# Kernel optimization log

Hardware: AMD Instinct MI355X
Metric: run time of the kernel (lower is better)

The kernel has to match this reference:

```python
import jax, jax.numpy as jnp
import numpy as np

LMAX = 2
C1 = 64; C2 = 64; COUT = 64
B = 4096
SUM_RDIM = sum(3**L for L in range(LMAX + 1))   # 13
FEAT1 = C1 * SUM_RDIM                            # 832
FEAT2 = C2 * SUM_RDIM


def _enumerate_paths(Lmax):
    paths = []
    for L1 in range(Lmax + 1):
        for L2 in range(Lmax + 1):
            for k in range(min(L1, L2) + 1):
                Lout = L1 + L2 - 2 * k
                if 0 <= Lout <= Lmax:
                    paths.append((L1, L2, Lout, k, False))
            if L1 >= 1 and L2 >= 1:
                for k in range(min(L1 - 1, L2 - 1) + 1):
                    Lout = L1 + L2 - 2 * k - 1
                    if 0 <= Lout <= Lmax:
                        paths.append((L1, L2, Lout, k, True))
    return paths

PATHS = _enumerate_paths(LMAX)   # 15 paths for Lmax=2


def _path_eq(L1, L2, k, use_eps):
    # Fused equation: W[c,a,b] contracted together with the delta/eps path einsum.
    letters = list('defghijklmnopqrstuvwxyz')  # a,b,c reserved for channels
    i_idx = letters[:L1]
    j_idx = letters[L1:L1 + L2]
    for r in range(k):  # delta: contract last k indices of A with last k of B
        j_idx[L2 - k + r] = i_idx[L1 - k + r]
    i_free = i_idx[:L1 - k]
    j_free = j_idx[:L2 - k]
    eps_sub = None
    if use_eps:  # consume last free index of each side via eps_{p i j}
        p = letters[L1 + L2]
        eps_sub = p + i_free[-1] + j_free[-1]
        i_free, j_free = i_free[:-1], j_free[:-1]
        out = i_free + j_free + [p]
    else:
        out = i_free + j_free
    terms = ['cab', '...a' + ''.join(i_idx), '...b' + ''.join(j_idx)]
    if eps_sub is not None:
        terms.append(eps_sub)
    return ','.join(terms) + '->...c' + ''.join(out)


def _epsilon():
    e = np.zeros((3, 3, 3), dtype=np.float32)
    e[0, 1, 2] = e[1, 2, 0] = e[2, 0, 1] = 1.0
    e[2, 1, 0] = e[1, 0, 2] = e[0, 2, 1] = -1.0
    return jnp.asarray(e)


def _split_by_rank(x, C, Lmax):
    batch = x.shape[:-1]
    out, idx = {}, 0
    for L in range(Lmax + 1):
        d = C * 3**L
        blk = x[..., idx:idx + d]
        idx += d
        out[L] = blk.reshape(*batch, C) if L == 0 else blk.reshape(*batch, C, *((3,) * L))
    return out


def setup_inputs() -> dict:
    key = jax.random.key(0)
    k1, k2, k3 = jax.random.split(key, 3)
    x1 = jax.random.normal(k1, (B, FEAT1), dtype=jnp.float32)
    x2 = jax.random.normal(k2, (B, FEAT2), dtype=jnp.float32)
    weight = jax.random.normal(k3, (len(PATHS) * COUT * C1 * C2,), dtype=jnp.float32) * 0.02
    return {"x1": x1, "x2": x2, "weight": weight}


def reference(x1, x2, weight):
    A = _split_by_rank(x1, C1, LMAX)
    Bt = _split_by_rank(x2, C2, LMAX)
    eps = _epsilon().astype(x1.dtype)
    batch = x1.shape[:-1]
    blocks = {L: jnp.zeros((*batch, COUT) + (3,) * L, dtype=x1.dtype) for L in range(LMAX + 1)}
    wsz = COUT * C1 * C2
    for n, (L1, L2, Lout, k, use_eps) in enumerate(PATHS):
        Wp = weight[n * wsz:(n + 1) * wsz].reshape(COUT, C1, C2)
        eq = _path_eq(L1, L2, k, use_eps)
        ops = (Wp, A[L1], Bt[L2]) + ((eps,) if use_eps else ())
        blocks[Lout] = blocks[Lout] + jnp.einsum(eq, *ops, optimize='optimal')
    parts = [blocks[L].reshape(*batch, COUT * 3**L) for L in range(LMAX + 1)]
    return jnp.concatenate(parts, axis=-1)
```

## Files before the change

kernel.cpp:

```cpp
#include <hip/hip_runtime.h>
#include <cstdint>
#include <cstddef>


#define FEAT 832
#define ZT 64

typedef _Float16 half8 __attribute__((ext_vector_type(8)));
typedef float floatx16 __attribute__((ext_vector_type(16)));

struct Chunk {
  int wbase;
  int o1[3];
  int o2[3];
  float sg[3];
  int d1, d2, nt;
};

__global__ void swz_w_kernel(const float* __restrict__ w, _Float16* __restrict__ o) {
  const int i = blockIdx.x * 256 + threadIdx.x;
  const int lane = i & 63;
  const int pkc  = i >> 6;
  const int cgrp = pkc & 1;
  const int ksg  = (pkc >> 1) & 255;
  const int p    = pkc >> 9;
  const int c  = cgrp * 32 + (lane & 31);
  const int k0 = ksg * 16 + (lane >> 5) * 8;
  const float* src = w + (size_t)p * 262144 + (size_t)c * 4096 + k0;
  const float4 v0 = *(const float4*)(src);
  const float4 v1 = *(const float4*)(src + 4);
  half8 h = { (_Float16)v0.x, (_Float16)v0.y, (_Float16)v0.z, (_Float16)v0.w,
              (_Float16)v1.x, (_Float16)v1.y, (_Float16)v1.z, (_Float16)v1.w };
  *(half8*)(o + (size_t)i * 8) = h;
}

template<int NT>
__device__ __forceinline__ void run_chunk(
    const Chunk C, const int zbase, const int zl, const int hf, const int lane,
    const int cgrp, const int tid,
    const float* __restrict__ x1, const float* __restrict__ x2,
    const _Float16* __restrict__ Wh, _Float16* __restrict__ XB,
    floatx16& acc)
{
  __syncthreads();

  #pragma unroll
  for (int t = 0; t < NT; ++t) {
    const size_t base2 = (size_t)zbase * FEAT + C.o2[t];
    for (int e = tid; e < 64 * 64; e += 256) {
      const int zz = e >> 6, b = e & 63;
      XB[(t * 64 + zz) * 72 + b] = (_Float16)x2[base2 + (size_t)zz * FEAT + b * C.d2];
    }
  }
  __syncthreads();

  half8 x2r[NT][4];
  #pragma unroll
  for (int t = 0; t < NT; ++t) {
    #pragma unroll
    for (int ks = 0; ks < 4; ++ks)
      x2r[t][ks] = *(const half8*)&XB[(t * 64 + zl) * 72 + ks * 16 + hf * 8];
  }
  __syncthreads();

  #pragma unroll
  for (int t = 0; t < NT; ++t) {
    const float sgf = C.sg[t];
    const int o1 = C.o1[t];
    for (int e = tid; e < 64 * 64; e += 256) {
      const int a = e & 63, zz = e >> 6;
      XB[(t * 64 + a) * 66 + zz] =
          (_Float16)(x1[(size_t)(zbase + zz) * FEAT + o1 + a * C.d1] * sgf);
    }
  }
  __syncthreads();

  const _Float16* __restrict__ Wp = Wh + C.wbase + cgrp * 512 + lane * 8;
  const _Float16* __restrict__ Xp = XB + zl;

  half8 af[4];
  #pragma unroll
  for (int ks = 0; ks < 4; ++ks)
    af[ks] = *(const half8*)(Wp + ks * 1024);

  for (int a = 0; a < 64; ++a) {
    half8 sv[NT];
    #pragma unroll
    for (int t = 0; t < NT; ++t) {
      const _Float16 h = Xp[(t * 64 + a) * 66];
      sv[t] = half8{h, h, h, h, h, h, h, h};
    }

    half8 afn[4];
    if (a < 63) {
      #pragma unroll
      for (int ks = 0; ks < 4; ++ks)
        afn[ks] = *(const half8*)(Wp + (a + 1) * 4096 + ks * 1024);
    }

    #pragma unroll
    for (int ks = 0; ks < 4; ++ks) {
      half8 tb = sv[0] * x2r[0][ks];
      if (NT > 1) tb += sv[1] * x2r[1][ks];
      if (NT > 2) tb += sv[2] * x2r[2][ks];
      acc = __builtin_amdgcn_mfma_f32_32x32x16_f16(af[ks], tb, acc, 0, 0, 0);
    }

    #pragma unroll
    for (int ks = 0; ks < 4; ++ks) af[ks] = afn[ks];
  }
}

__global__ __launch_bounds__(256, 3) void tp_kernel(
    const float* __restrict__ x1, const float* __restrict__ x2,
    const _Float16* __restrict__ Wh, float* __restrict__ out)
{
  __shared__ __align__(16) _Float16 XB[3 * 64 * 72];
  __shared__ Chunk chs[7];
  __shared__ int nch_s;

  const int tid  = threadIdx.x;
  const int slot = blockIdx.y;
  const int zbase = blockIdx.x * ZT;
  const int wv   = tid >> 6;
  const int lane = tid & 63;
  const int ln31 = lane & 31;
  const int hf   = lane >> 5;
  const int zgrp = wv & 1;
  const int cgrp = wv >> 1;
  const int zl   = zgrp * 32 + ln31;
  const int zg   = zbase + zl;

  int offO, dO, mO;
  if (slot == 0)      { offO = 0;   dO = 1; mO = 0; }
  else if (slot < 4)  { offO = 64;  dO = 3; mO = slot - 1; }
  else                { offO = 256; dO = 9; mO = slot - 4; }

  if (tid == 0) {
    int n = 0;
    auto add = [&](int p, int L1, int L2,
                   int i0, int i1, int i2, int j0, int j1, int j2,
                   float s0, float s1, float s2, int nt) {
      const int offs[3] = {0, 64, 256};
      const int ds[3]   = {1, 3, 9};
      Chunk c;
      c.wbase = p * 262144;
      c.o1[0] = offs[L1] + i0; c.o1[1] = offs[L1] + i1; c.o1[2] = offs[L1] + i2;
      c.o2[0] = offs[L2] + j0; c.o2[1] = offs[L2] + j1; c.o2[2] = offs[L2] + j2;
      c.sg[0] = s0; c.sg[1] = s1; c.sg[2] = s2;
      c.d1 = ds[L1]; c.d2 = ds[L2]; c.nt = nt;
      chs[n++] = c;
    };
    if (slot == 0) {
      add(0, 0,0, 0,0,0, 0,0,0, 1,0,0, 1);
      add(5, 1,1, 0,1,2, 0,1,2, 1,1,1, 3);
      add(13,2,2, 0,1,2, 0,1,2, 1,1,1, 3);
      add(13,2,2, 3,4,5, 3,4,5, 1,1,1, 3);
      add(13,2,2, 6,7,8, 6,7,8, 1,1,1, 3);
    } else if (slot < 4) {
      const int m = slot - 1, p1 = (m+1)%3, p2 = (m+2)%3;
      add(1, 0,1, 0,0,0, m,0,0, 1,0,0, 1);
      add(3, 1,0, m,0,0, 0,0,0, 1,0,0, 1);
      add(6, 1,1, p1,p2,0, p2,p1,0, 1,-1,0, 2);
      add(7, 1,2, 0,1,2, 3*m,3*m+1,3*m+2, 1,1,1, 3);
      add(10,2,1, 3*m,3*m+1,3*m+2, 0,1,2, 1,1,1, 3);
      add(14,2,2, 3*p1,3*p1+1,3*p1+2, 3*p2,3*p2+1,3*p2+2, 1,1,1, 3);
      add(14,2,2, 3*p2,3*p2+1,3*p2+2, 3*p1,3*p1+1,3*p1+2, -1,-1,-1, 3);
    } else {
      const int m = slot - 4, u = m/3, v = m%3, q1 = (v+1)%3, q2 = (v+2)%3;
      add(2, 0,2, 0,0,0, m,0,0, 1,0,0, 1);
      add(4, 1,1, u,0,0, v,0,0, 1,0,0, 1);
      add(8, 1,2, q1,q2,0, 3*u+q2,3*u+q1,0, 1,-1,0, 2);
      add(9, 2,0, m,0,0, 0,0,0, 1,0,0, 1);
      add(11,2,1, 3*u+q1,3*u+q2,0, q2,q1,0, 1,-1,0, 2);
      add(12,2,2, 3*u,3*u+1,3*u+2, 3*v,3*v+1,3*v+2, 1,1,1, 3);
    }
    nch_s = n;
  }
  __syncthreads();
  const int nch = nch_s;

  floatx16 acc;
  #pragma unroll
  for (int r = 0; r < 16; ++r) acc[r] = 0.0f;

  for (int ci = 0; ci < nch; ++ci) {
    const Chunk C = chs[ci];
    if (C.nt == 1)      run_chunk<1>(C, zbase, zl, hf, lane, cgrp, tid, x1, x2, Wh, XB, acc);
    else if (C.nt == 2) run_chunk<2>(C, zbase, zl, hf, lane, cgrp, tid, x1, x2, Wh, XB, acc);
    else                run_chunk<3>(C, zbase, zl, hf, lane, cgrp, tid, x1, x2, Wh, XB, acc);
  }

  float* __restrict__ op = out + (size_t)zg * FEAT + offO + mO;
  #pragma unroll
  for (int r = 0; r < 16; ++r) {
    const int cr = (r & 3) + 8 * (r >> 2) + 4 * hf + cgrp * 32;
    op[(size_t)cr * dO] = acc[r];
  }
}

extern "C" void kernel_launch(void* const* d_in, const int* in_sizes, int n_in,
                              void* d_out, int out_size, void* d_ws, size_t ws_size,
                              hipStream_t stream) {
  const float* x1 = (const float*)d_in[0];
  const float* x2 = (const float*)d_in[1];
  const float* w  = (const float*)d_in[2];
  float* out = (float*)d_out;
  _Float16* Wh = (_Float16*)d_ws;

  const int nchunks = 15 * 64 * 4096 / 8;
  hipLaunchKernelGGL(swz_w_kernel, dim3(nchunks / 256), dim3(256), 0, stream, w, Wh);

  dim3 grid(64, 13);
  hipLaunchKernelGGL(tp_kernel, grid, dim3(256), 0, stream, x1, x2, Wh, out);
}
```

Baseline: 434.3 us.

## Halve block to two waves, each covering both z-halves to reuse weight fragments

The block shrinks from four waves to two. Each wave now computes two 32-row z tiles with two accumulators, so every weight fragment loaded from global memory feeds two MFMAs and per-wave weight traffic is halved. x1 and x2 are staged into separate LDS buffers, which removes one barrier and lets the A-scale values be prefetched one iteration ahead. Global loads of x are marked nontemporal. The cost is more registers per wave (two accumulators, doubled x2 fragments), fewer threads for LDS staging, and fewer waves per block to hide latency.

```diff
diff --git a/kernel.cpp b/kernel.cpp
--- a/kernel.cpp
+++ b/kernel.cpp
@@ -34,102 +34,117 @@
   *(half8*)(o + (size_t)i * 8) = h;
 }
 
+__device__ __forceinline__ half8 splat8(_Float16 h) {
+  return half8{h, h, h, h, h, h, h, h};
+}
+
 template<int NT>
 __device__ __forceinline__ void run_chunk(
-    const Chunk C, const int zbase, const int zl, const int hf, const int lane,
-    const int cgrp, const int tid,
+    const Chunk C, const int zbase, const int ln31, const int hf,
+    const int cgrp, const int lane, const int tid,
     const float* __restrict__ x1, const float* __restrict__ x2,
-    const _Float16* __restrict__ Wh, _Float16* __restrict__ XB,
-    floatx16& acc)
+    const _Float16* __restrict__ Wh,
+    _Float16* __restrict__ XS2, _Float16* __restrict__ XS1,
+    floatx16& acc0, floatx16& acc1)
 {
   __syncthreads();
 
   #pragma unroll
   for (int t = 0; t < NT; ++t) {
     const size_t base2 = (size_t)zbase * FEAT + C.o2[t];
-    for (int e = tid; e < 64 * 64; e += 256) {
+    #pragma unroll
+    for (int e = tid; e < 64 * 64; e += 128) {
       const int zz = e >> 6, b = e & 63;
-      XB[(t * 64 + zz) * 72 + b] = (_Float16)x2[base2 + (size_t)zz * FEAT + b * C.d2];
-    }
-  }
-  __syncthreads();
-
-  half8 x2r[NT][4];
-  #pragma unroll
-  for (int t = 0; t < NT; ++t) {
-    #pragma unroll
-    for (int ks = 0; ks < 4; ++ks)
-      x2r[t][ks] = *(const half8*)&XB[(t * 64 + zl) * 72 + ks * 16 + hf * 8];
-  }
-  __syncthreads();
-
+      XS2[(t * 64 + zz) * 72 + b] =
+          (_Float16)__builtin_nontemporal_load(&x2[base2 + (size_t)zz * FEAT + b * C.d2]);
+    }
+  }
   #pragma unroll
   for (int t = 0; t < NT; ++t) {
     const float sgf = C.sg[t];
     const int o1 = C.o1[t];
-    for (int e = tid; e < 64 * 64; e += 256) {
+    #pragma unroll
+    for (int e = tid; e < 64 * 64; e += 128) {
       const int a = e & 63, zz = e >> 6;
-      XB[(t * 64 + a) * 66 + zz] =
-          (_Float16)(x1[(size_t)(zbase + zz) * FEAT + o1 + a * C.d1] * sgf);
+      XS1[(t * 64 + a) * 65 + zz] =
+          (_Float16)(__builtin_nontemporal_load(&x1[(size_t)(zbase + zz) * FEAT + o1 + a * C.d1]) * sgf);
     }
   }
   __syncthreads();
 
-  const _Float16* __restrict__ Wp = Wh + C.wbase + cgrp * 512 + lane * 8;
-  const _Float16* __restrict__ Xp = XB + zl;
+  half8 x2r0[NT][4], x2r1[NT][4];
+  #pragma unroll
+  for (int t = 0; t < NT; ++t) {
+    #pragma unroll
+    for (int ks = 0; ks < 4; ++ks) {
+      x2r0[t][ks] = *(const half8*)&XS2[(t * 64 + ln31) * 72 + ks * 16 + hf * 8];
+      x2r1[t][ks] = *(const half8*)&XS2[(t * 64 + 32 + ln31) * 72 + ks * 16 + hf * 8];
+    }
+  }
+
+  const _Float16* __restrict__ Wq = Wh + C.wbase + cgrp * 512 + lane * 8;
 
   half8 af[4];
   #pragma unroll
-  for (int ks = 0; ks < 4; ++ks)
-    af[ks] = *(const half8*)(Wp + ks * 1024);
+  for (int ks = 0; ks < 4; ++ks) af[ks] = *(const half8*)(Wq + ks * 1024);
+  _Float16 sc0[NT], sc1[NT];
+  #pragma unroll
+  for (int t = 0; t < NT; ++t) {
+    sc0[t] = XS1[(t * 64 + 0) * 65 + ln31];
+    sc1[t] = XS1[(t * 64 + 0) * 65 + 32 + ln31];
+  }
 
   for (int a = 0; a < 64; ++a) {
-    half8 sv[NT];
-    #pragma unroll
-    for (int t = 0; t < NT; ++t) {
-      const _Float16 h = Xp[(t * 64 + a) * 66];
-      sv[t] = half8{h, h, h, h, h, h, h, h};
-    }
-
     half8 afn[4];
+    _Float16 scn0[NT], scn1[NT];
     if (a < 63) {
       #pragma unroll
       for (int ks = 0; ks < 4; ++ks)
-        afn[ks] = *(const half8*)(Wp + (a + 1) * 4096 + ks * 1024);
-    }
+        afn[ks] = *(const half8*)(Wq + (a + 1) * 4096 + ks * 1024);
+      #pragma unroll
+      for (int t = 0; t < NT; ++t) {
+        scn0[t] = XS1[(t * 64 + a + 1) * 65 + ln31];
+        scn1[t] = XS1[(t * 64 + a + 1) * 65 + 32 + ln31];
+      }
+    }
+
+    half8 sv0[NT], sv1[NT];
+    #pragma unroll
+    for (int t = 0; t < NT; ++t) { sv0[t] = splat8(sc0[t]); sv1[t] = splat8(sc1[t]); }
 
     #pragma unroll
     for (int ks = 0; ks < 4; ++ks) {
-      half8 tb = sv[0] * x2r[0][ks];
-      if (NT > 1) tb += sv[1] * x2r[1][ks];
-      if (NT > 2) tb += sv[2] * x2r[2][ks];
-      acc = __builtin_amdgcn_mfma_f32_32x32x16_f16(af[ks], tb, acc, 0, 0, 0);
+      half8 tb0 = sv0[0] * x2r0[0][ks];
+      half8 tb1 = sv1[0] * x2r1[0][ks];
+      if (NT > 1) { tb0 += sv0[1] * x2r0[1][ks]; tb1 += sv1[1] * x2r1[1][ks]; }
+      if (NT > 2) { tb0 += sv0[2] * x2r0[2][ks]; tb1 += sv1[2] * x2r1[2][ks]; }
+      acc0 = __builtin_amdgcn_mfma_f32_32x32x16_f16(af[ks], tb0, acc0, 0, 0, 0);
+      acc1 = __builtin_amdgcn_mfma_f32_32x32x16_f16(af[ks], tb1, acc1, 0, 0, 0);
     }
 
     #pragma unroll
     for (int ks = 0; ks < 4; ++ks) af[ks] = afn[ks];
-  }
-}
-
-__global__ __launch_bounds__(256, 3) void tp_kernel(
+    #pragma unroll
+    for (int t = 0; t < NT; ++t) { sc0[t] = scn0[t]; sc1[t] = scn1[t]; }
+  }
+}
+
+__global__ __launch_bounds__(128, 2) void tp_kernel(
     const float* __restrict__ x1, const float* __restrict__ x2,
     const _Float16* __restrict__ Wh, float* __restrict__ out)
 {
-  __shared__ __align__(16) _Float16 XB[3 * 64 * 72];
+  __shared__ __align__(16) _Float16 XS2[3 * 64 * 72];
+  __shared__ __align__(16) _Float16 XS1[3 * 64 * 65];
   __shared__ Chunk chs[7];
   __shared__ int nch_s;
 
   const int tid  = threadIdx.x;
   const int slot = blockIdx.y;
   const int zbase = blockIdx.x * ZT;
-  const int wv   = tid >> 6;
+  const int cgrp = tid >> 6;
   const int lane = tid & 63;
   const int ln31 = lane & 31;
   const int hf   = lane >> 5;
-  const int zgrp = wv & 1;
-  const int cgrp = wv >> 1;
-  const int zl   = zgrp * 32 + ln31;
-  const int zg   = zbase + zl;
 
   int offO, dO, mO;
   if (slot == 0)      { offO = 0;   dO = 1; mO = 0; }
@@ -180,22 +195,24 @@
   __syncthreads();
   const int nch = nch_s;
 
-  floatx16 acc;
-  #pragma unroll
-  for (int r = 0; r < 16; ++r) acc[r] = 0.0f;
+  floatx16 acc0, acc1;
+  #pragma unroll
+  for (int r = 0; r < 16; ++r) { acc0[r] = 0.0f; acc1[r] = 0.0f; }
 
   for (int ci = 0; ci < nch; ++ci) {
     const Chunk C = chs[ci];
-    if (C.nt == 1)      run_chunk<1>(C, zbase, zl, hf, lane, cgrp, tid, x1, x2, Wh, XB, acc);
-    else if (C.nt == 2) run_chunk<2>(C, zbase, zl, hf, lane, cgrp, tid, x1, x2, Wh, XB, acc);
-    else                run_chunk<3>(C, zbase, zl, hf, lane, cgrp, tid, x1, x2, Wh, XB, acc);
-  }
-
-  float* __restrict__ op = out + (size_t)zg * FEAT + offO + mO;
+    if (C.nt == 1)      run_chunk<1>(C, zbase, ln31, hf, cgrp, lane, tid, x1, x2, Wh, XS2, XS1, acc0, acc1);
+    else if (C.nt == 2) run_chunk<2>(C, zbase, ln31, hf, cgrp, lane, tid, x1, x2, Wh, XS2, XS1, acc0, acc1);
+    else                run_chunk<3>(C, zbase, ln31, hf, cgrp, lane, tid, x1, x2, Wh, XS2, XS1, acc0, acc1);
+  }
+
+  float* __restrict__ op0 = out + (size_t)(zbase + ln31) * FEAT + offO + mO;
+  float* __restrict__ op1 = out + (size_t)(zbase + 32 + ln31) * FEAT + offO + mO;
   #pragma unroll
   for (int r = 0; r < 16; ++r) {
     const int cr = (r & 3) + 8 * (r >> 2) + 4 * hf + cgrp * 32;
-    op[(size_t)cr * dO] = acc[r];
+    op0[(size_t)cr * dO] = acc0[r];
+    op1[(size_t)cr * dO] = acc1[r];
   }
 }
 
@@ -212,5 +229,5 @@
   hipLaunchKernelGGL(swz_w_kernel, dim3(nchunks / 256), dim3(256), 0, stream, w, Wh);
 
   dim3 grid(64, 13);
-  hipLaunchKernelGGL(tp_kernel, grid, dim3(256), 0, stream, x1, x2, Wh, out);
-}
+  hipLaunchKernelGGL(tp_kernel, grid, dim3(128), 0, stream, x1, x2, Wh, out);
+}
```

New measurement: 957.2 us. 120% more time.
